# Kernel tuning notes

Hardware: AMD Instinct MI355X
Metric: run time of the kernel (lower is better)

## Reference

```python
import jax, jax.numpy as jnp
import numpy as np

N_QUBITS = 10
BATCH = 16384
Q_DEPTH = 2


def _apply_1q_shared(state, U, q):
    # state: [B, 2, 2, ..., 2]; U: [2, 2] complex, acting on wire q
    state = jnp.moveaxis(state, 1 + q, -1)
    state = jnp.einsum('b...i,ji->b...j', state, U)
    return jnp.moveaxis(state, -1, 1 + q)


def _apply_ry_batched(state, angles, q):
    # per-sample RY(angle) on wire q; angles: [B] float
    c = jnp.cos(angles * 0.5).astype(jnp.complex64)
    s = jnp.sin(angles * 0.5).astype(jnp.complex64)
    U = jnp.stack([jnp.stack([c, -s], -1), jnp.stack([s, c], -1)], -2)  # [B,2,2]
    state = jnp.moveaxis(state, 1 + q, -1)
    state = jnp.einsum('b...i,bji->b...j', state, U)
    return jnp.moveaxis(state, -1, 1 + q)


def _rot_matrix(phi, theta, omega):
    # PennyLane Rot = RZ(omega) @ RY(theta) @ RZ(phi)
    c = jnp.cos(theta * 0.5)
    s = jnp.sin(theta * 0.5)
    m00 = jnp.exp(-0.5j * (phi + omega)) * c
    m01 = -jnp.exp(0.5j * (phi - omega)) * s
    m10 = jnp.exp(-0.5j * (phi - omega)) * s
    m11 = jnp.exp(0.5j * (phi + omega)) * c
    return jnp.stack([jnp.stack([m00, m01]), jnp.stack([m10, m11])]).astype(jnp.complex64)


def _apply_cnot(state, c, t):
    st = jnp.moveaxis(state, (1 + c, 1 + t), (1, 2))  # [B, ctrl, tgt, ...]
    st = jnp.stack([st[:, 0], st[:, 1, ::-1]], axis=1)  # flip target where ctrl=1
    return jnp.moveaxis(st, (1, 2), (1 + c, 1 + t))


def setup_inputs() -> dict:
    key = jax.random.key(0)
    k1, k2 = jax.random.split(key)
    x = jax.random.uniform(k1, (BATCH, N_QUBITS), dtype=jnp.float32) * np.pi
    q_weights = 0.01 * jax.random.normal(k2, (Q_DEPTH, N_QUBITS, 3), dtype=jnp.float32)
    return {"x": x, "q_weights": q_weights}


def reference(x, q_weights) -> jnp.ndarray:
    B, n = x.shape
    L = q_weights.shape[0]
    # |0...0> statevector, batched: [B] + [2]*n (axis q <-> wire q, wire 0 most significant)
    state = jnp.zeros((B, 2 ** n), jnp.complex64).at[:, 0].set(1.0)
    state = state.reshape((B,) + (2,) * n)
    # AngleEmbedding(rotation='Y')
    for q in range(n):
        state = _apply_ry_batched(state, x[:, q], q)
    # StronglyEntanglingLayers: Rot on each wire, then ring of CNOTs with range (l % (n-1)) + 1
    for l in range(L):
        for q in range(n):
            U = _rot_matrix(q_weights[l, q, 0], q_weights[l, q, 1], q_weights[l, q, 2])
            state = _apply_1q_shared(state, U, q)
        r = (l % (n - 1)) + 1
        for q in range(n):
            state = _apply_cnot(state, q, (q + r) % n)
    probs = jnp.abs(state.reshape(B, 2 ** n)) ** 2  # [B, 2^n]
    bits = (np.arange(2 ** n)[:, None] >> (n - 1 - np.arange(n))[None, :]) & 1
    signs = jnp.asarray(1.0 - 2.0 * bits, jnp.float32)  # [2^n, n], PauliZ eigenvalues
    return (probs @ signs).astype(jnp.float32)  # [B, n] expvals
```

## Files before the change

### kernel.cpp

```cpp
#include <hip/hip_runtime.h>

#define DEVINL __device__ __forceinline__

typedef float f32x2 __attribute__((ext_vector_type(2)));

struct GC { int laneXor, regXor, rowL, rowR; };
struct Circ { GC g[20]; int sgnL[10], sgnR[10]; int lsel[5]; };

constexpr Circ build_circ() {
    Circ c{};
    unsigned A[10] = {};
    for (int i = 0; i < 10; ++i) A[i] = 1u << i;
    for (int w = 0; w < 10; ++w) {
        int pos = 9 - w;
        unsigned m = 1u << pos;
        c.g[w] = GC{ int(m >> 5), int(m & 31u), int(m >> 5), int(m & 31u) };
    }
    for (int q = 0; q < 10; ++q) { int pc = 9 - q, pt = 9 - ((q + 1) % 10); A[pt] ^= A[pc]; }
    unsigned M[10] = {}, Inv[10] = {};
    for (int i = 0; i < 10; ++i) { M[i] = A[i]; Inv[i] = 1u << i; }
    for (int col = 0; col < 10; ++col) {
        int piv = col;
        while (!((M[piv] >> col) & 1u)) ++piv;
        unsigned tm = M[col]; M[col] = M[piv]; M[piv] = tm;
        unsigned ti = Inv[col]; Inv[col] = Inv[piv]; Inv[piv] = ti;
        for (int r = 0; r < 10; ++r)
            if (r != col && ((M[r] >> col) & 1u)) { M[r] ^= M[col]; Inv[r] ^= Inv[col]; }
    }
    for (int w = 0; w < 10; ++w) {
        int pos = 9 - w;
        unsigned m = 0;
        for (int i = 0; i < 10; ++i) m |= ((Inv[i] >> pos) & 1u) << i;
        unsigned row = A[pos];
        c.g[10 + w] = GC{ int(m >> 5), int(m & 31u), int(row >> 5), int(row & 31u) };
    }
    for (int q = 0; q < 10; ++q) { int pc = 9 - q, pt = 9 - ((q + 2) % 10); A[pt] ^= A[pc]; }
    for (int q = 0; q < 10; ++q) { unsigned row = A[9 - q]; c.sgnL[q] = int(row >> 5); c.sgnR[q] = int(row & 31u); }

    unsigned Ucols[5] = {};
    {
        unsigned tgt[5] = {16, 8, 2, 12, 1};
        unsigned acc = 0;
        for (int k = 0; k < 5; ++k) { acc ^= tgt[k]; Ucols[k] = acc; }
    }
    unsigned Urows[5] = {};
    for (int r = 0; r < 5; ++r)
        for (int cc = 0; cc < 5; ++cc)
            Urows[r] |= ((Ucols[cc] >> r) & 1u) << cc;
    unsigned MM[5] = {}, AI[5] = {};
    for (int i = 0; i < 5; ++i) { MM[i] = Urows[i]; AI[i] = 1u << i; }
    for (int col = 0; col < 5; ++col) {
        int piv = col;
        while (!((MM[piv] >> col) & 1u)) ++piv;
        unsigned tm = MM[col]; MM[col] = MM[piv]; MM[piv] = tm;
        unsigned ti = AI[col]; AI[col] = AI[piv]; AI[piv] = ti;
        for (int r = 0; r < 5; ++r)
            if (r != col && ((MM[r] >> col) & 1u)) { MM[r] ^= MM[col]; AI[r] ^= AI[col]; }
    }
    for (int w = 0; w < 10; ++w) {
        unsigned mL = unsigned(c.g[10 + w].laneXor);
        unsigned nm = 0;
        for (int i = 0; i < 5; ++i) if ((mL >> i) & 1u) nm ^= Ucols[i];
        c.g[10 + w].laneXor = int(nm);
        unsigned rL = unsigned(c.g[10 + w].rowL);
        unsigned nr = 0;
        for (int i = 0; i < 5; ++i) if ((rL >> i) & 1u) nr ^= AI[i];
        c.g[10 + w].rowL = int(nr);
    }
    for (int q = 0; q < 10; ++q) {
        unsigned sL = unsigned(c.sgnL[q]);
        unsigned ns = 0;
        for (int i = 0; i < 5; ++i) if ((sL >> i) & 1u) ns ^= AI[i];
        c.sgnL[q] = int(ns);
    }
    for (int o = 0; o < 5; ++o) c.lsel[o] = int(AI[o]);
    return c;
}

constexpr Circ CC = build_circ();

static_assert(CC.g[10].laneXor == 1  && CC.g[10].regXor == 0,  "w0");
static_assert(CC.g[11].laneXor == 12 && CC.g[11].regXor == 0,  "w1");
static_assert(CC.g[12].laneXor == 2  && CC.g[12].regXor == 0,  "w2");
static_assert(CC.g[13].laneXor == 8  && CC.g[13].regXor == 0,  "w3");
static_assert(CC.g[14].laneXor == 16 && CC.g[14].regXor == 16, "w4");
static_assert(CC.g[15].laneXor == 0  && CC.g[15].regXor == 24, "w5");
static_assert(CC.g[16].laneXor == 0  && CC.g[16].regXor == 12, "w6");
static_assert(CC.g[17].laneXor == 0  && CC.g[17].regXor == 6,  "w7");
static_assert(CC.g[18].laneXor == 0  && CC.g[18].regXor == 3,  "w8");
static_assert(CC.g[19].laneXor == 1  && CC.g[19].regXor == 1,  "w9");
static_assert(CC.g[10].rowR == 31, "w0 rowR");
static_assert(CC.g[11].rowR == 0,  "w1 rowR");
static_assert(CC.g[12].rowR == 0,  "w2 rowR");
static_assert(CC.g[13].rowR == 0,  "w3 rowR");
static_assert(CC.g[14].rowR == 0,  "w4 rowR");
static_assert(CC.g[15].rowR == 16, "w5 rowR");
static_assert(CC.g[16].rowR == 24, "w6 rowR");
static_assert(CC.g[17].rowR == 28, "w7 rowR");
static_assert(CC.g[18].rowR == 30, "w8 rowR");
static_assert(CC.g[19].rowR == 31, "w9 rowR");

DEVINL float csw(float v, int sw) {
    return __int_as_float(__float_as_int(v) ^ sw);
}
DEVINL int sgnw(int l5, int rowL) {
    return (__popc(unsigned(l5 & rowL)) & 1) << 31;
}

template<int XOR>
DEVINL float fetch(float v) {
    if constexpr (XOR == 0)      return v;
    else if constexpr (XOR == 1) return __int_as_float(__builtin_amdgcn_update_dpp(0, __float_as_int(v), 0xB1, 0xF, 0xF, true));
    else if constexpr (XOR == 2) return __int_as_float(__builtin_amdgcn_update_dpp(0, __float_as_int(v), 0x4E, 0xF, 0xF, true));
    else if constexpr (XOR == 3) return __int_as_float(__builtin_amdgcn_update_dpp(0, __float_as_int(v), 0x1B, 0xF, 0xF, true));
    else if constexpr (XOR == 8) return __int_as_float(__builtin_amdgcn_update_dpp(0, __float_as_int(v), 0x128, 0xF, 0xF, true));
    else                         return __int_as_float(__builtin_amdgcn_ds_swizzle(__float_as_int(v), 0x1F | (XOR << 10)));
}

DEVINL void pk_fma_acc(f32x2& a, f32x2 t, f32x2 b) {
    asm("v_pk_fma_f32 %0, %1, %2, %0" : "+v"(a) : "v"(t), "v"(b));
}

DEVINL f32x2 cmul(f32x2 a, f32x2 b) {
    f32x2 r;
    r.x = a.x * b.x - a.y * b.y;
    r.y = a.x * b.y + a.y * b.x;
    return r;
}

__device__ __attribute__((aligned(16))) float g_cst[80];

__global__ void qprep(const float* __restrict__ qw) {
    int g = threadIdx.x;
    if (g < 10) {
        float phi = qw[g * 3 + 0], th = qw[g * 3 + 1], om = qw[g * 3 + 2];
        float c = cosf(0.5f * th), s = sinf(0.5f * th);
        float apo = 0.5f * (phi + om), amo = 0.5f * (phi - om);
        g_cst[g * 4 + 0] =  cosf(apo) * c;
        g_cst[g * 4 + 1] = -sinf(apo) * c;
        g_cst[g * 4 + 2] = -cosf(amo) * s;
        g_cst[g * 4 + 3] = -sinf(amo) * s;
    } else if (g < 20) {
        int w = g - 10;
        float phi = qw[g * 3 + 0], th = qw[g * 3 + 1];
        float c = cosf(0.5f * th), s = sinf(0.5f * th);
        g_cst[40 + w] = s / c;
        g_cst[50 + w * 2 + 0] =  cosf(0.5f * phi);
        g_cst[50 + w * 2 + 1] = -sinf(0.5f * phi);
    } else if (g == 20) {
        float p = 1.f;
        for (int w = 0; w < 10; ++w) p *= cosf(0.5f * qw[(10 + w) * 3 + 1]);
        g_cst[70] = p;
    }
}

DEVINL f32x2 mkE(const float* cst, int w, int l5) {
    f32x2 E;
    E.x = cst[50 + w * 2];
    E.y = csw(cst[50 + w * 2 + 1], sgnw(l5, CC.g[10 + w].rowL));
    return E;
}

DEVINL void wf(const float* cst, float xw, int w, f32x2& f0, f32x2& f1) {
    float h = 0.5f * xw;
    float s = __sinf(h), c = __cosf(h);
    float m0 = cst[w * 4 + 0], m1 = cst[w * 4 + 1], m2 = cst[w * 4 + 2], m3 = cst[w * 4 + 3];
    f0.x =  m0 * c + m2 * s;
    f0.y =  m1 * c + m3 * s;
    f1.x = -m2 * c + m0 * s;
    f1.y =  m3 * c - m1 * s;
}

template<int W>
DEVINL void apply_gate(f32x2 (&a2)[32], const float* cst, int l5) {
    constexpr GC gc = CC.g[10 + W];
    float tt = csw(cst[40 + W], sgnw(l5, gc.rowL));
    f32x2 tp; tp.x = tt;  tp.y = tt;
    f32x2 tn; tn.x = -tt; tn.y = -tt;
    if constexpr (gc.laneXor == 0) {
        #pragma unroll
        for (int r = 0; r < 32; ++r) {
            const int r2 = r ^ gc.regXor;
            if (r < r2) {
                const bool sR  = __builtin_popcount(unsigned(gc.rowR & r )) & 1;
                const bool sR2 = __builtin_popcount(unsigned(gc.rowR & r2)) & 1;
                f32x2 ca = a2[r], cb = a2[r2];
                f32x2 na = ca + (sR  ? tp : tn) * cb;
                f32x2 nb = cb + (sR2 ? tp : tn) * ca;
                a2[r] = na; a2[r2] = nb;
            }
        }
    } else if constexpr (gc.regXor == 0) {
        #pragma unroll
        for (int r = 0; r < 32; ++r) {
            f32x2 b;
            b.x = fetch<gc.laneXor>(a2[r].x);
            b.y = fetch<gc.laneXor>(a2[r].y);
            const bool sR = __builtin_popcount(unsigned(gc.rowR & r)) & 1;
            pk_fma_acc(a2[r], sR ? tp : tn, b);
        }
    } else {
        #pragma unroll
        for (int r = 0; r < 32; ++r) {
            const int r2 = r ^ gc.regXor;
            if (r < r2) {
                f32x2 blo, bhi;
                blo.x = fetch<gc.laneXor>(a2[r2].x);
                blo.y = fetch<gc.laneXor>(a2[r2].y);
                bhi.x = fetch<gc.laneXor>(a2[r].x);
                bhi.y = fetch<gc.laneXor>(a2[r].y);
                const bool sR  = __builtin_popcount(unsigned(gc.rowR & r )) & 1;
                const bool sR2 = __builtin_popcount(unsigned(gc.rowR & r2)) & 1;
                pk_fma_acc(a2[r],  sR  ? tp : tn, blo);
                pk_fma_acc(a2[r2], sR2 ? tp : tn, bhi);
            }
        }
    }
}

__global__ __launch_bounds__(256) void qsim(const float* __restrict__ x,
                                            float* __restrict__ out, int B) {
    const float* cst = g_cst;
    int lane = threadIdx.x & 63;
    int l5 = lane & 31;
    int b = blockIdx.x * 8 + (threadIdx.x >> 5);
    if (b >= B) return;

    const f32x2* xp = reinterpret_cast<const f32x2*>(x + b * 10);
    f32x2 xv0 = xp[0], xv1 = xp[1], xv2 = xp[2], xv3 = xp[3], xv4 = xp[4];
    float xw[10] = { xv0.x, xv0.y, xv1.x, xv1.y, xv2.x,
                     xv2.y, xv3.x, xv3.y, xv4.x, xv4.y };

    f32x2 t01[4], t23[4], f5t[2];
    {
        f32x2 a0, a1, b0, b1;
        wf(cst, xw[9], 9, a0, a1);
        wf(cst, xw[8], 8, b0, b1);
        t01[0] = cmul(a0, b0); t01[1] = cmul(a1, b0);
        t01[2] = cmul(a0, b1); t01[3] = cmul(a1, b1);
        wf(cst, xw[7], 7, a0, a1);
        wf(cst, xw[6], 6, b0, b1);
        t23[0] = cmul(a0, b0); t23[1] = cmul(a1, b0);
        t23[2] = cmul(a0, b1); t23[3] = cmul(a1, b1);
        wf(cst, xw[5], 5, f5t[0], f5t[1]);
    }

    f32x2 lf;
    {
        f32x2 p0, p1, p2, p3, p4;
        {
            f32x2 f0, f1;
            wf(cst, xw[4], 4, f0, f1);
            int bit = __popc(unsigned(l5 & CC.lsel[0])) & 1;
            p0.x = bit ? f1.x : f0.x;  p0.y = bit ? f1.y : f0.y;
            wf(cst, xw[3], 3, f0, f1);
            bit = __popc(unsigned(l5 & CC.lsel[1])) & 1;
            p1.x = bit ? f1.x : f0.x;  p1.y = bit ? f1.y : f0.y;
            wf(cst, xw[2], 2, f0, f1);
            bit = __popc(unsigned(l5 & CC.lsel[2])) & 1;
            p2.x = bit ? f1.x : f0.x;  p2.y = bit ? f1.y : f0.y;
            wf(cst, xw[1], 1, f0, f1);
            bit = __popc(unsigned(l5 & CC.lsel[3])) & 1;
            p3.x = bit ? f1.x : f0.x;  p3.y = bit ? f1.y : f0.y;
            wf(cst, xw[0], 0, f0, f1);
            bit = __popc(unsigned(l5 & CC.lsel[4])) & 1;
            p4.x = bit ? f1.x : f0.x;  p4.y = bit ? f1.y : f0.y;
        }
        f32x2 pl = cmul(cmul(cmul(p0, p1), cmul(p2, p3)), p4);
        f32x2 ea = mkE(cst, 1, l5);
        ea = cmul(ea, mkE(cst, 2, l5));
        ea = cmul(ea, mkE(cst, 3, l5));
        ea = cmul(ea, mkE(cst, 4, l5));
        float sc = cst[70];
        ea.x *= sc; ea.y *= sc;
        lf = cmul(pl, ea);
    }

    f32x2 f5p[2], V00, V01, H0, H1;
    {
        f32x2 E5 = mkE(cst, 5, l5);
        f5p[0] = cmul(f5t[0], E5);
        E5.y = -E5.y;
        f5p[1] = cmul(f5t[1], E5);
        f32x2 E6 = mkE(cst, 6, l5), E7 = mkE(cst, 7, l5);
        V00 = cmul(E6, E7);
        E7.y = -E7.y;
        V01 = cmul(E6, E7);
        f32x2 EB = cmul(mkE(cst, 9, l5), mkE(cst, 0, l5));
        f32x2 E8 = mkE(cst, 8, l5);
        H0 = cmul(E8, EB);
        EB.y = -EB.y;
        H1 = cmul(E8, EB);
    }

    f32x2 g4H[4][2];
    #pragma unroll
    for (int v = 0; v < 4; ++v) {
        f32x2 g = cmul(lf, t01[v]);
        f32x2 H = (v & 1) ? H1 : H0;
        g4H[v][0] = cmul(g, H);
        f32x2 Hc; Hc.x = H.x; Hc.y = -H.y;
        g4H[v][1] = cmul(g, Hc);
    }

    f32x2 a2[32];
    #pragma unroll
    for (int j = 0; j < 8; ++j) {
        f32x2 tA = cmul(t23[j & 3], f5p[j >> 2]);
        const int s6 = ((j >> 2) ^ (j >> 1)) & 1;
        const int s7 = s6 ^ (j & 1);
        f32x2 V;
        V.x = s6 ? (s7 ? V00.x : V01.x) : (s7 ? V01.x : V00.x);
        V.y = s6 ? -(s7 ? V00.y : V01.y) : (s7 ? V01.y : V00.y);
        f32x2 tfj = cmul(tA, V);
        const int pj = __builtin_popcount(unsigned(j)) & 1;
        #pragma unroll
        for (int v = 0; v < 4; ++v) {
            const int sel = ((v >> 1) ^ pj) & 1;
            a2[(j << 2) | v] = cmul(g4H[v][sel], tfj);
        }
    }

    apply_gate<4>(a2, cst, l5);
    apply_gate<5>(a2, cst, l5);
    apply_gate<3>(a2, cst, l5);
    apply_gate<6>(a2, cst, l5);
    apply_gate<1>(a2, cst, l5);
    apply_gate<7>(a2, cst, l5);
    apply_gate<2>(a2, cst, l5);
    apply_gate<8>(a2, cst, l5);
    apply_gate<0>(a2, cst, l5);
    apply_gate<9>(a2, cst, l5);

    float wv[32];
    #pragma unroll
    for (int r = 0; r < 32; ++r) wv[r] = a2[r].x * a2[r].x + a2[r].y * a2[r].y;
    #pragma unroll
    for (int bS = 1; bS < 16; bS <<= 1) {
        #pragma unroll
        for (int r = 0; r < 32; ++r) {
            if (!(r & bS)) {
                float xvv = wv[r], yv = wv[r | bS];
                wv[r]      = xvv + yv;
                wv[r | bS] = xvv - yv;
            }
        }
    }

    float e[10];
    #pragma unroll
    for (int q = 0; q < 10; ++q) {
        const int R = CC.sgnR[q];
        float num = (R & 16) ? (wv[R ^ 16] - wv[R]) : (wv[R] + wv[R ^ 16]);
        int slq = __popc(unsigned(l5 & CC.sgnL[q])) & 1;
        e[q] = csw(num, slq << 31);
    }

    #pragma unroll
    for (int q = 0; q < 10; ++q) {
        e[q] += fetch<1>(e[q]);
        e[q] += fetch<2>(e[q]);
    }
    int s = l5 & 3;
    bool s1 = (s & 1) != 0, s2 = (s & 2) != 0;
    float v0 = s1 ? e[1] : e[0];
    float u0 = s1 ? e[3] : e[2];
    v0 = s2 ? u0 : v0;
    float v1 = s1 ? e[5] : e[4];
    float u1 = s1 ? e[7] : e[6];
    v1 = s2 ? u1 : v1;
    float v2 = s1 ? e[9] : e[8];

    v0 += fetch<4>(v0);   v1 += fetch<4>(v1);   v2 += fetch<4>(v2);
    v0 += fetch<8>(v0);   v1 += fetch<8>(v1);   v2 += fetch<8>(v2);
    v0 += fetch<16>(v0);  v1 += fetch<16>(v1);  v2 += fetch<16>(v2);

    float vo = v0;
    int hi = l5 >> 2;
    vo = (hi == 1) ? v1 : vo;
    vo = (hi == 2) ? v2 : vo;
    if (l5 < 10) out[b * 10 + l5] = vo;
}

extern "C" void kernel_launch(void* const* d_in, const int* in_sizes, int n_in,
                              void* d_out, int out_size, void* d_ws, size_t ws_size,
                              hipStream_t stream) {
    const float* x  = (const float*)d_in[0];
    const float* qw = (const float*)d_in[1];
    float* out = (float*)d_out;
    int B = in_sizes[0] / 10;
    int blocks = (B + 7) / 8;
    hipLaunchKernelGGL(qprep, dim3(1), dim3(64), 0, stream, qw);
    hipLaunchKernelGGL(qsim, dim3(blocks), dim3(256), 0, stream, x, out, B);
}
```

Measured before the change: 81.86 us.

## Apply three layer-two gates on factored product state before full expansion

Measured after the change: 80.32 us. No clear change (-1.9%).

```diff
diff --git a/kernel.cpp b/kernel.cpp
--- a/kernel.cpp
+++ b/kernel.cpp
@@ -303,7 +303,7 @@
         g4H[v][1] = cmul(g, Hc);
     }
 
-    f32x2 a2[32];
+    f32x2 tf[8];
     #pragma unroll
     for (int j = 0; j < 8; ++j) {
         f32x2 tA = cmul(t23[j & 3], f5p[j >> 2]);
@@ -312,23 +312,70 @@
         f32x2 V;
         V.x = s6 ? (s7 ? V00.x : V01.x) : (s7 ? V01.x : V00.x);
         V.y = s6 ? -(s7 ? V00.y : V01.y) : (s7 ? V01.y : V00.y);
-        f32x2 tfj = cmul(tA, V);
-        const int pj = __builtin_popcount(unsigned(j)) & 1;
+        tf[j] = cmul(tA, V);
+    }
+
+    {
+        float t5 = csw(cst[40 + 5], sgnw(l5, CC.g[15].rowL));
+        f32x2 tp; tp.x = t5;  tp.y = t5;
+        f32x2 tn; tn.x = -t5; tn.y = -t5;
+        #pragma unroll
+        for (int j = 0; j < 8; ++j) {
+            const int j2 = j ^ 6;
+            if (j < j2) {
+                f32x2 ca = tf[j], cb = tf[j2];
+                tf[j]  = ca + (((j  >> 2) & 1) ? tp : tn) * cb;
+                tf[j2] = cb + (((j2 >> 2) & 1) ? tp : tn) * ca;
+            }
+        }
+    }
+    {
+        float t6 = csw(cst[40 + 6], sgnw(l5, CC.g[16].rowL));
+        f32x2 tp; tp.x = t6;  tp.y = t6;
+        f32x2 tn; tn.x = -t6; tn.y = -t6;
+        #pragma unroll
+        for (int j = 0; j < 8; ++j) {
+            const int j2 = j ^ 3;
+            if (j < j2) {
+                const bool sA = (((j  >> 1) ^ (j  >> 2)) & 1);
+                const bool sB = (((j2 >> 1) ^ (j2 >> 2)) & 1);
+                f32x2 ca = tf[j], cb = tf[j2];
+                tf[j]  = ca + (sA ? tp : tn) * cb;
+                tf[j2] = cb + (sB ? tp : tn) * ca;
+            }
+        }
+    }
+    f32x2 g4Hp[4][2];
+    {
+        float t8 = csw(cst[40 + 8], sgnw(l5, CC.g[18].rowL));
+        f32x2 tp; tp.x = t8;  tp.y = t8;
+        f32x2 tn; tn.x = -t8; tn.y = -t8;
         #pragma unroll
         for (int v = 0; v < 4; ++v) {
-            const int sel = ((v >> 1) ^ pj) & 1;
-            a2[(j << 2) | v] = cmul(g4H[v][sel], tfj);
+            #pragma unroll
+            for (int P = 0; P < 2; ++P) {
+                const int sel = ((v >> 1) ^ P) & 1;
+                const bool sg = ((((v >> 1) & 1) ^ P) & 1);
+                g4Hp[v][P] = g4H[v][sel] + (sg ? tp : tn) * g4H[v ^ 3][sel ^ 1];
+            }
+        }
+    }
+
+    f32x2 a2[32];
+    #pragma unroll
+    for (int j = 0; j < 8; ++j) {
+        const int pj = (j ^ (j >> 1) ^ (j >> 2)) & 1;
+        #pragma unroll
+        for (int v = 0; v < 4; ++v) {
+            a2[(j << 2) | v] = cmul(g4Hp[v][pj], tf[j]);
         }
     }
 
     apply_gate<4>(a2, cst, l5);
-    apply_gate<5>(a2, cst, l5);
+    apply_gate<7>(a2, cst, l5);
     apply_gate<3>(a2, cst, l5);
-    apply_gate<6>(a2, cst, l5);
     apply_gate<1>(a2, cst, l5);
-    apply_gate<7>(a2, cst, l5);
     apply_gate<2>(a2, cst, l5);
-    apply_gate<8>(a2, cst, l5);
     apply_gate<0>(a2, cst, l5);
     apply_gate<9>(a2, cst, l5);
 
```
